# Performance work log

Hardware: AMD Instinct MI355X
Metric: run time of the kernel (lower is better)

Reference implementation:

```python
import jax, jax.numpy as jnp
import numpy as np

B, S, D, H = 4, 2048, 1024, 16
HD = D // H
DFF = 4 * D
EPS = 1e-5


def setup_inputs() -> dict:
    key = jax.random.key(0)
    ks = jax.random.split(key, 8)
    s = 0.02
    return {
        "x": jax.random.normal(ks[0], (B, S, D), dtype=jnp.float32),
        "ln1_g": jnp.ones((D,), jnp.float32),
        "ln1_b": jnp.zeros((D,), jnp.float32),
        "Wq": jax.random.normal(ks[1], (D, D), jnp.float32) * s,
        "Wk": jax.random.normal(ks[2], (D, D), jnp.float32) * s,
        "Wv": jax.random.normal(ks[3], (D, D), jnp.float32) * s,
        "Wo": jax.random.normal(ks[4], (D, D), jnp.float32) * s,
        "ln2_g": jnp.ones((D,), jnp.float32),
        "ln2_b": jnp.zeros((D,), jnp.float32),
        "W1": jax.random.normal(ks[5], (D, DFF), jnp.float32) * s,
        "b1": jnp.zeros((DFF,), jnp.float32),
        "W2": jax.random.normal(ks[6], (DFF, D), jnp.float32) * s,
        "b2": jnp.zeros((D,), jnp.float32),
    }


def _layernorm(x, g, b):
    mu = jnp.mean(x, axis=-1, keepdims=True)
    var = jnp.var(x, axis=-1, keepdims=True)
    return (x - mu) * jax.lax.rsqrt(var + EPS) * g + b


def _block(x, ln1_g, ln1_b, Wq, Wk, Wv, Wo, ln2_g, ln2_b, W1, b1, W2, b2):
    # --- attention sub-block (pre-norm) ---
    h = _layernorm(x, ln1_g, ln1_b)
    q = (h @ Wq).reshape(B, S, H, HD)
    k = (h @ Wk).reshape(B, S, H, HD)
    v = (h @ Wv).reshape(B, S, H, HD)
    scores = jnp.einsum("bqhd,bkhd->bhqk", q, k) / np.sqrt(HD).astype(np.float32)
    causal = jnp.tril(jnp.ones((S, S), dtype=bool))
    scores = jnp.where(causal, scores, -jnp.inf)
    attn = jax.nn.softmax(scores, axis=-1)  # dropout p=0 (eval)
    ctx = jnp.einsum("bhqk,bkhd->bqhd", attn, v).reshape(B, S, D)
    x = x + ctx @ Wo
    # --- FFN sub-block (pre-norm) ---
    h = _layernorm(x, ln2_g, ln2_b)
    h = jax.nn.gelu(h @ W1 + b1, approximate=False)  # torch nn.GELU() = exact erf
    return x + (h @ W2 + b2)


def reference(x, ln1_g, ln1_b, Wq, Wk, Wv, Wo, ln2_g, ln2_b, W1, b1, W2, b2):
    return _block(x, ln1_g, ln1_b, Wq, Wk, Wv, Wo, ln2_g, ln2_b, W1, b1, W2, b2)
```

## Files before the change

### kernel.cpp

```cpp
#include <hip/hip_runtime.h>
#include <hip/hip_bf16.h>
#include <math.h>

#define NB 4
#define NS 2048
#define ND 1024
#define NH 16
#define NHD 64
#define NDFF 4096
#define QKS 3072

typedef __attribute__((ext_vector_type(8))) short bf16x8;
typedef __attribute__((ext_vector_type(4))) float f32x4;
typedef __attribute__((ext_vector_type(16))) float f32x16;
typedef __attribute__((ext_vector_type(4))) short short4v;
typedef __attribute__((ext_vector_type(4))) int i32x4;

static __device__ __forceinline__ short f2b(float f) {
  union { __hip_bfloat16 b; short s; } u;
  u.b = __float2bfloat16(f);
  return u.s;
}

static __device__ __forceinline__ int cvtpk(float lo, float hi_) {
  int r;
  asm("v_cvt_pk_bf16_f32 %0, %1, %2" : "=v"(r) : "v"(lo), "v"(hi_));
  return r;
}

static __device__ __forceinline__ float pairmax(float x) {
  auto r = __builtin_amdgcn_permlane32_swap(__float_as_uint(x), __float_as_uint(x), false, false);
  return fmaxf(__uint_as_float(r[0]), __uint_as_float(r[1]));
}
static __device__ __forceinline__ float pairsum(float x) {
  auto r = __builtin_amdgcn_permlane32_swap(__float_as_uint(x), __float_as_uint(x), false, false);
  return __uint_as_float(r[0]) + __uint_as_float(r[1]);
}

__global__ __launch_bounds__(256) void ln_kernel(
    const float* __restrict__ x, const float* __restrict__ g,
    const float* __restrict__ b, short* __restrict__ out) {
  __shared__ float red[8];
  const int row = blockIdx.x;
  const int t = threadIdx.x;
  const float* xr = x + (size_t)row * ND;
  const float4 xv = *(const float4*)(xr + t * 4);
  float s = xv.x + xv.y + xv.z + xv.w;
  float ss = xv.x * xv.x + xv.y * xv.y + xv.z * xv.z + xv.w * xv.w;
#pragma unroll
  for (int m = 32; m >= 1; m >>= 1) {
    s += __shfl_xor(s, m);
    ss += __shfl_xor(ss, m);
  }
  if ((t & 63) == 0) { red[(t >> 6) * 2] = s; red[(t >> 6) * 2 + 1] = ss; }
  __syncthreads();
  s = red[0] + red[2] + red[4] + red[6];
  ss = red[1] + red[3] + red[5] + red[7];
  const float mu = s * (1.0f / ND);
  const float var = ss * (1.0f / ND) - mu * mu;
  const float rs = rsqrtf(var + 1e-5f);
  const float4 gv = *(const float4*)(g + t * 4);
  const float4 bv = *(const float4*)(b + t * 4);
  short o[4];
  o[0] = f2b((xv.x - mu) * rs * gv.x + bv.x);
  o[1] = f2b((xv.y - mu) * rs * gv.y + bv.y);
  o[2] = f2b((xv.z - mu) * rs * gv.z + bv.z);
  o[3] = f2b((xv.w - mu) * rs * gv.w + bv.w);
  *(short4v*)(out + (size_t)row * ND + t * 4) = *(short4v*)o;
}

__global__ __launch_bounds__(256) void tcast_kernel(
    const float* __restrict__ in, short* __restrict__ out, int K, int N) {
  __shared__ float tile[32][33];
  const int n0 = blockIdx.x * 32, k0 = blockIdx.y * 32;
  const int tx = threadIdx.x & 31, ty = threadIdx.x >> 5;
#pragma unroll
  for (int i = 0; i < 32; i += 8)
    tile[ty + i][tx] = in[(size_t)(k0 + ty + i) * N + n0 + tx];
  __syncthreads();
#pragma unroll
  for (int i = 0; i < 32; i += 8)
    out[(size_t)(n0 + ty + i) * K + k0 + tx] = f2b(tile[tx][ty + i]);
}

__global__ __launch_bounds__(256) void vtrans_kernel(
    const short* __restrict__ in, short* __restrict__ out) {
  __shared__ short tile[64][72];
  const int s0 = blockIdx.x * 64, bh = blockIdx.y;
  const int bb = bh >> 4, hh = bh & 15;
  const int rr = threadIdx.x >> 3, cc = (threadIdx.x & 7) * 8;
#pragma unroll
  for (int it = 0; it < 2; ++it) {
    const int r = rr + it * 32;
    *(bf16x8*)&tile[r][cc] =
        *(const bf16x8*)&in[((size_t)(bb * NS + s0 + r)) * QKS + 2048 + hh * NHD + cc];
  }
  __syncthreads();
  const size_t ob = (size_t)bh * NHD * NS;
#pragma unroll
  for (int it = 0; it < 2; ++it) {
    const int d = rr + it * 32;
    short o[8];
#pragma unroll
    for (int j = 0; j < 8; ++j) o[j] = tile[cc + j][d];
    *(bf16x8*)&out[ob + (size_t)d * NS + s0 + cc] = *(bf16x8*)o;
  }
}

__device__ __forceinline__ void gload16(const void* g, void* l) {
  __builtin_amdgcn_global_load_lds(
      (const __attribute__((address_space(1))) unsigned int*)g,
      (__attribute__((address_space(3))) unsigned int*)l, 16, 0, 0);
}

template <int BN, int EPI>
__global__ __launch_bounds__(BN * 2, 2) void gemmk_kernel(
    const short* __restrict__ A, const short* __restrict__ Bt,
    float* __restrict__ Cf, short* __restrict__ Cb,
    const float* __restrict__ bias, const float* __restrict__ res,
    int M, int N, int K) {
  constexpr int WN = BN / 64;
  constexpr int T = 128 * WN;
  constexpr int AROUNDS = 1024 / T;
  constexpr int BROUNDS = 2;
  constexpr int TS = (256 + BN) * 32;
  __shared__ short lds[3][TS];

  const int tid = threadIdx.x;
  const int l = tid & 63, w = tid >> 6;
  const int wm = w / WN, wn = w % WN;
  const int nbm = M >> 8, nbn = N / BN, nwg = nbm * nbn;
  int wg = blockIdx.x;
  wg = (wg & 7) * (nwg >> 3) + (wg >> 3);
  const int bm = wg % nbm, bn = wg / nbm;

  const int srcs = (l & 3) ^ ((l >> 2) & 3) ^ ((l >> 4) & 3);
  const short* Asrc = A + (size_t)(bm * 256 + (tid >> 2)) * K + srcs * 8;
  const short* Bsrc = Bt + (size_t)(bn * BN + (tid >> 2)) * K + srcs * 8;

  auto stage = [&](int u, int sb) {
    short* d = &lds[sb][0] + w * 512;
    const short* as = Asrc + u * 32;
    const short* bs = Bsrc + u * 32;
#pragma unroll
    for (int j = 0; j < AROUNDS; ++j)
      gload16(as + (size_t)j * (T / 4) * K, d + j * T * 8);
#pragma unroll
    for (int j = 0; j < BROUNDS; ++j)
      gload16(bs + (size_t)j * (T / 4) * K, d + 8192 + j * T * 8);
  };

  const int fr = l & 15, fg4 = l >> 4;
  int aoff[8], boff[4];
#pragma unroll
  for (int mi = 0; mi < 8; ++mi) {
    const int r = wm * 128 + mi * 16 + fr;
    aoff[mi] = r * 32 + (fg4 ^ (r & 3) ^ ((r >> 2) & 3)) * 8;
  }
#pragma unroll
  for (int nj = 0; nj < 4; ++nj) {
    const int r = wn * 64 + nj * 16 + fr;
    boff[nj] = 8192 + r * 32 + (fg4 ^ (r & 3) ^ ((r >> 2) & 3)) * 8;
  }

  f32x4 acc[8][4] = {};
  const int NT = K >> 5;
  stage(0, 0);
  stage(1, 1);
  int rb = 0;
  for (int t = 0; t < NT; ++t) {
    if (t + 1 < NT) {
      if constexpr (BN == 256)
        asm volatile("s_waitcnt vmcnt(4)\n\ts_barrier" ::: "memory");
      else
        asm volatile("s_waitcnt vmcnt(6)\n\ts_barrier" ::: "memory");
    } else {
      asm volatile("s_waitcnt vmcnt(0)\n\ts_barrier" ::: "memory");
    }
    if (t + 2 < NT) {
      int sb = rb + 2;
      if (sb >= 3) sb -= 3;
      stage(t + 2, sb);
    }
    const short* la = &lds[rb][0];
    bf16x8 af[8], bf[4];
#pragma unroll
    for (int mi = 0; mi < 8; ++mi) af[mi] = *(const bf16x8*)(la + aoff[mi]);
#pragma unroll
    for (int nj = 0; nj < 4; ++nj) bf[nj] = *(const bf16x8*)(la + boff[nj]);
    __builtin_amdgcn_s_setprio(1);
#pragma unroll
    for (int mi = 0; mi < 8; ++mi)
#pragma unroll
      for (int nj = 0; nj < 4; ++nj)
        acc[mi][nj] = __builtin_amdgcn_mfma_f32_16x16x32_bf16(af[mi], bf[nj], acc[mi][nj], 0, 0, 0);
    __builtin_amdgcn_s_setprio(0);
    if (++rb == 3) rb = 0;
  }

  const int fq = (l >> 4) * 4;
  const int wrb = bm * 256 + wm * 128;
  const int wcb = bn * BN + wn * 64;
#pragma unroll
  for (int mi = 0; mi < 8; ++mi) {
#pragma unroll
    for (int ni = 0; ni < 4; ++ni) {
#pragma unroll
      for (int rr = 0; rr < 4; ++rr) {
        const int row = wrb + mi * 16 + fq + rr;
        const int col = wcb + ni * 16 + fr;
        float v = acc[mi][ni][rr];
        if (EPI == 0) {
          Cb[(size_t)row * N + col] = f2b(v);
        } else if (EPI == 1) {
          Cf[(size_t)row * N + col] = v + res[(size_t)row * N + col];
        } else if (EPI == 2) {
          v += bias[col];
          v = 0.5f * v * (1.0f + erff(v * 0.70710678118f));
          Cb[(size_t)row * N + col] = f2b(v);
        } else {
          Cf[(size_t)row * N + col] = v + bias[col] + res[(size_t)row * N + col];
        }
      }
    }
  }
}

__global__ __launch_bounds__(256, 2) void attn_kernel(
    const short* __restrict__ qkv, const short* __restrict__ vt, short* __restrict__ ctx) {
  __shared__ short Kls[2][64 * 64];
  __shared__ short Vls[2][64 * 64];

  const int bid = blockIdx.x;
  const int bh = (bid & 7) * 8 + ((bid >> 3) & 7);
  const int cp = bid >> 6;
  const int bb = bh >> 4, hh = bh & 15;
  const int lane = threadIdx.x & 63, wave = threadIdx.x >> 6;
  const int ql = lane & 31, hi = lane >> 5;
  const int qbA = cp * 128 + wave * 32;
  const int qbB = (15 - cp) * 128 + wave * 32;

  bf16x8 qf[2][4];
#pragma unroll
  for (int hf = 0; hf < 2; ++hf) {
    const int qb0 = hf ? qbB : qbA;
    const size_t qrow = ((size_t)bb * NS + qb0 + ql) * QKS + hh * NHD;
#pragma unroll
    for (int st = 0; st < 4; ++st)
      qf[hf][st] = *(const bf16x8*)&qkv[qrow + st * 16 + hi * 8];
  }

  f32x16 acc[2][2] = {};
  float m_run[2] = {-1e37f, -1e37f};
  float l_run[2] = {0.f, 0.f};

  const int srow = lane >> 3;
  const int sslot = (lane & 7) ^ srow;
  const short* kbasep = qkv + (size_t)bb * NS * QKS + 1024 + hh * NHD + sslot * 8;
  const short* vbasep = vt + (size_t)bh * NHD * NS + sslot * 8;

  const int nkt = (16 - cp) * 2;
#pragma unroll
  for (int r = 0; r < 2; ++r) {
    const int row = r * 32 + wave * 8 + srow;
    gload16(kbasep + (size_t)row * QKS, &Kls[0][(r * 32 + wave * 8) * 64]);
    gload16(vbasep + (size_t)row * NS, &Vls[0][(r * 32 + wave * 8) * 64]);
  }

  int buf = 0;
  for (int jt = 0; jt < nkt; ++jt) {
    asm volatile("s_waitcnt vmcnt(0)\n\ts_barrier" ::: "memory");
    if (jt + 1 < nkt) {
      const int k0n = (jt + 1) * 64;
#pragma unroll
      for (int r = 0; r < 2; ++r) {
        const int row = r * 32 + wave * 8 + srow;
        gload16(kbasep + (size_t)(k0n + row) * QKS, &Kls[buf ^ 1][(r * 32 + wave * 8) * 64]);
        gload16(vbasep + (size_t)row * NS + k0n, &Vls[buf ^ 1][(r * 32 + wave * 8) * 64]);
      }
    }
    const int k0 = jt * 64;
    const short* Kb = &Kls[buf][0];
    const short* Vb = &Vls[buf][0];
#pragma unroll
    for (int ks = 0; ks < 2; ++ks) {
      const int kbase = k0 + ks * 32;
      if (kbase > qbB) continue;
      bf16x8 kf[4], vf[2][2];
      const int krow = ks * 32 + ql;
#pragma unroll
      for (int st = 0; st < 4; ++st)
        kf[st] = *(const bf16x8*)&Kb[krow * 64 + ((st * 2 + hi) ^ (krow & 7)) * 8];
#pragma unroll
      for (int db = 0; db < 2; ++db) {
        const int vrow = db * 32 + ql;
#pragma unroll
        for (int su = 0; su < 2; ++su)
          vf[db][su] =
              *(const bf16x8*)&Vb[vrow * 64 + ((ks * 4 + su * 2 + hi) ^ (vrow & 7)) * 8];
      }
#pragma unroll
      for (int hf = 0; hf < 2; ++hf) {
        const int qb0 = hf ? qbB : qbA;
        if (kbase > qb0) continue;
        const int qg = qb0 + ql;
        f32x16 s = {};
        __builtin_amdgcn_s_setprio(1);
#pragma unroll
        for (int st = 0; st < 4; ++st)
          s = __builtin_amdgcn_mfma_f32_32x32x16_bf16(kf[st], qf[hf][st], s, 0, 0, 0);
        __builtin_amdgcn_s_setprio(0);
        const bool masked = (kbase + 31 > qb0);
        float pv[16];
        float mt = -INFINITY;
#pragma unroll
        for (int r = 0; r < 16; ++r) {
          float v = s[r] * 0.125f;
          if (masked) {
            const int key = kbase + 4 * hi + (r & 3) + 8 * (r >> 2);
            v = (key > qg) ? -INFINITY : v;
          }
          pv[r] = v;
          mt = fmaxf(mt, v);
        }
        mt = pairmax(mt);
        if (!__all(mt - m_run[hf] <= 8.0f)) {
          const float mn = fmaxf(m_run[hf], mt);
          const float sc = __expf(m_run[hf] - mn);
          m_run[hf] = mn;
          l_run[hf] *= sc;
          acc[hf][0] *= sc;
          acc[hf][1] *= sc;
        }
        float pe[16];
        float lt = 0.f;
#pragma unroll
        for (int r = 0; r < 16; ++r) {
          pe[r] = __expf(fminf(pv[r] - m_run[hf], 80.0f));
          lt += pe[r];
        }
        l_run[hf] += pairsum(lt);
        bf16x8 pf[2];
#pragma unroll
        for (int su = 0; su < 2; ++su) {
          const int a0 = cvtpk(pe[su * 8 + 0], pe[su * 8 + 1]);
          const int a1 = cvtpk(pe[su * 8 + 2], pe[su * 8 + 3]);
          const int b0 = cvtpk(pe[su * 8 + 4], pe[su * 8 + 5]);
          const int b1 = cvtpk(pe[su * 8 + 6], pe[su * 8 + 7]);
          auto r0 = __builtin_amdgcn_permlane32_swap((unsigned)a0, (unsigned)b0, false, false);
          auto r1 = __builtin_amdgcn_permlane32_swap((unsigned)a1, (unsigned)b1, false, false);
          union { i32x4 w; bf16x8 v; } u;
          u.w[0] = r0[0]; u.w[1] = r1[0]; u.w[2] = r0[1]; u.w[3] = r1[1];
          pf[su] = u.v;
        }
        __builtin_amdgcn_s_setprio(1);
#pragma unroll
        for (int su = 0; su < 2; ++su) {
          acc[hf][0] = __builtin_amdgcn_mfma_f32_32x32x16_bf16(vf[0][su], pf[su], acc[hf][0], 0, 0, 0);
          acc[hf][1] = __builtin_amdgcn_mfma_f32_32x32x16_bf16(vf[1][su], pf[su], acc[hf][1], 0, 0, 0);
        }
        __builtin_amdgcn_s_setprio(0);
      }
    }
    asm volatile("s_waitcnt lgkmcnt(0)\n\ts_barrier" ::: "memory");
    buf ^= 1;
  }

#pragma unroll
  for (int hf = 0; hf < 2; ++hf) {
    const int qb0 = hf ? qbB : qbA;
    const float inv = 1.0f / l_run[hf];
    const size_t ob = ((size_t)bb * NS + qb0 + ql) * ND + hh * NHD + hi * 8;
#pragma unroll
    for (int db = 0; db < 2; ++db) {
#pragma unroll
      for (int J = 0; J < 2; ++J) {
        const int a0 = cvtpk(acc[hf][db][J * 8 + 0] * inv, acc[hf][db][J * 8 + 1] * inv);
        const int a1 = cvtpk(acc[hf][db][J * 8 + 2] * inv, acc[hf][db][J * 8 + 3] * inv);
        const int b0 = cvtpk(acc[hf][db][J * 8 + 4] * inv, acc[hf][db][J * 8 + 5] * inv);
        const int b1 = cvtpk(acc[hf][db][J * 8 + 6] * inv, acc[hf][db][J * 8 + 7] * inv);
        auto r0 = __builtin_amdgcn_permlane32_swap((unsigned)a0, (unsigned)b0, false, false);
        auto r1 = __builtin_amdgcn_permlane32_swap((unsigned)a1, (unsigned)b1, false, false);
        union { i32x4 w; bf16x8 v; } u;
        u.w[0] = r0[0]; u.w[1] = r1[0]; u.w[2] = r0[1]; u.w[3] = r1[1];
        *(bf16x8*)&ctx[ob + db * 32 + J * 16] = u.v;
      }
    }
  }
}

extern "C" void kernel_launch(void* const* d_in, const int* in_sizes, int n_in,
                              void* d_out, int out_size, void* d_ws, size_t ws_size,
                              hipStream_t stream) {
  (void)in_sizes; (void)n_in; (void)out_size; (void)ws_size;
  const float* x     = (const float*)d_in[0];
  const float* ln1_g = (const float*)d_in[1];
  const float* ln1_b = (const float*)d_in[2];
  const float* Wq    = (const float*)d_in[3];
  const float* Wk    = (const float*)d_in[4];
  const float* Wv    = (const float*)d_in[5];
  const float* Wo    = (const float*)d_in[6];
  const float* ln2_g = (const float*)d_in[7];
  const float* ln2_b = (const float*)d_in[8];
  const float* W1    = (const float*)d_in[9];
  const float* b1    = (const float*)d_in[10];
  const float* W2    = (const float*)d_in[11];
  const float* b2    = (const float*)d_in[12];
  float* out = (float*)d_out;

  char* ws = (char*)d_ws;
  const size_t MiB = 1024 * 1024;
  short* wqkvT = (short*)(ws + 0 * MiB);
  short* woT   = (short*)(ws + 6 * MiB);
  short* w1T   = (short*)(ws + 8 * MiB);
  short* w2T   = (short*)(ws + 16 * MiB);
  short* h     = (short*)(ws + 24 * MiB);
  short* ctx   = (short*)(ws + 24 * MiB);
  short* qkv   = (short*)(ws + 40 * MiB);
  short* vt    = (short*)(ws + 88 * MiB);
  short* hff   = (short*)(ws + 40 * MiB);
  float* x1    = (float*)(ws + 104 * MiB);

  tcast_kernel<<<dim3(32, 32), 256, 0, stream>>>(Wq, wqkvT, 1024, 1024);
  tcast_kernel<<<dim3(32, 32), 256, 0, stream>>>(Wk, wqkvT + 1024 * 1024, 1024, 1024);
  tcast_kernel<<<dim3(32, 32), 256, 0, stream>>>(Wv, wqkvT + 2048 * 1024, 1024, 1024);
  tcast_kernel<<<dim3(32, 32), 256, 0, stream>>>(Wo, woT, 1024, 1024);
  tcast_kernel<<<dim3(128, 32), 256, 0, stream>>>(W1, w1T, 1024, 4096);
  tcast_kernel<<<dim3(32, 128), 256, 0, stream>>>(W2, w2T, 4096, 1024);

  ln_kernel<<<8192, 256, 0, stream>>>(x, ln1_g, ln1_b, h);

  gemmk_kernel<256, 0><<<384, 512, 0, stream>>>(h, wqkvT, nullptr, qkv, nullptr, nullptr,
                                                8192, 3072, 1024);
  vtrans_kernel<<<dim3(32, 64), 256, 0, stream>>>(qkv, vt);

  attn_kernel<<<512, 256, 0, stream>>>(qkv, vt, ctx);

  gemmk_kernel<128, 1><<<256, 256, 0, stream>>>(ctx, woT, x1, nullptr, nullptr, x,
                                                8192, 1024, 1024);

  ln_kernel<<<8192, 256, 0, stream>>>(x1, ln2_g, ln2_b, h);

  gemmk_kernel<256, 2><<<512, 512, 0, stream>>>(h, w1T, nullptr, hff, b1, nullptr,
                                                8192, 4096, 1024);
  gemmk_kernel<128, 3><<<256, 256, 0, stream>>>(hff, w2T, out, nullptr, b2, x1,
                                                8192, 1024, 4096);
}
```

Before: 427.0 us.

## Restructure GEMM mainloop into double-buffered K=64 ping-pong with interleaved prefetch

```diff
diff --git a/kernel.cpp b/kernel.cpp
--- a/kernel.cpp
+++ b/kernel.cpp
@@ -114,17 +114,18 @@
 }
 
 template <int BN, int EPI>
-__global__ __launch_bounds__(BN * 2, 2) void gemmk_kernel(
+__global__ __launch_bounds__(BN == 256 ? 512 : 256, BN == 256 ? 2 : 1) void gemmp_kernel(
     const short* __restrict__ A, const short* __restrict__ Bt,
     float* __restrict__ Cf, short* __restrict__ Cb,
     const float* __restrict__ bias, const float* __restrict__ res,
     int M, int N, int K) {
   constexpr int WN = BN / 64;
-  constexpr int T = 128 * WN;
-  constexpr int AROUNDS = 1024 / T;
-  constexpr int BROUNDS = 2;
-  constexpr int TS = (256 + BN) * 32;
-  __shared__ short lds[3][TS];
+  constexpr int TPB = WN * 128;
+  constexpr int ARNDS = 16384 / (TPB * 16);
+  constexpr int BSZ = BN * 32;
+  constexpr int SZ = 16384 + BN * 64;
+  constexpr int CNT = (BN == 256) ? 4 : 6;
+  __shared__ short lds[2][SZ];
 
   const int tid = threadIdx.x;
   const int l = tid & 63, w = tid >> 6;
@@ -134,42 +135,84 @@
   wg = (wg & 7) * (nwg >> 3) + (wg >> 3);
   const int bm = wg % nbm, bn = wg / nbm;
 
-  const int srcs = (l & 3) ^ ((l >> 2) & 3) ^ ((l >> 4) & 3);
-  const short* Asrc = A + (size_t)(bm * 256 + (tid >> 2)) * K + srcs * 8;
-  const short* Bsrc = Bt + (size_t)(bn * BN + (tid >> 2)) * K + srcs * 8;
-
-  auto stage = [&](int u, int sb) {
-    short* d = &lds[sb][0] + w * 512;
-    const short* as = Asrc + u * 32;
-    const short* bs = Bsrc + u * 32;
-#pragma unroll
-    for (int j = 0; j < AROUNDS; ++j)
-      gload16(as + (size_t)j * (T / 4) * K, d + j * T * 8);
-#pragma unroll
-    for (int j = 0; j < BROUNDS; ++j)
-      gload16(bs + (size_t)j * (T / 4) * K, d + 8192 + j * T * 8);
+  const int lrow0 = w * 16 + (l >> 2);
+  const int sslot = (l & 3) ^ ((lrow0 >> 1) & 3);
+  const short* Asrc = A + (size_t)(bm * 256 + lrow0) * K + sslot * 8;
+  const short* Bsrc = Bt + (size_t)(bn * BN + lrow0) * K + sslot * 8;
+
+  auto stageA = [&](int u, int kh, short* bufb) {
+    short* d = bufb + kh * 8192 + w * 512;
+    const short* s = Asrc + (size_t)u * 64 + kh * 32;
+#pragma unroll
+    for (int j = 0; j < ARNDS; ++j)
+      gload16(s + (size_t)j * (TPB / 4) * K, d + j * TPB * 8);
   };
+  auto stageB = [&](int u, int kh, short* bufb) {
+    short* d = bufb + 16384 + kh * BSZ + w * 512;
+    const short* s = Bsrc + (size_t)u * 64 + kh * 32;
+#pragma unroll
+    for (int j = 0; j < 2; ++j)
+      gload16(s + (size_t)j * (TPB / 4) * K, d + j * TPB * 8);
+  };
 
   const int fr = l & 15, fg4 = l >> 4;
-  int aoff[8], boff[4];
+  int aoffs[8], boffs[4];
 #pragma unroll
   for (int mi = 0; mi < 8; ++mi) {
     const int r = wm * 128 + mi * 16 + fr;
-    aoff[mi] = r * 32 + (fg4 ^ (r & 3) ^ ((r >> 2) & 3)) * 8;
-  }
-#pragma unroll
-  for (int nj = 0; nj < 4; ++nj) {
-    const int r = wn * 64 + nj * 16 + fr;
-    boff[nj] = 8192 + r * 32 + (fg4 ^ (r & 3) ^ ((r >> 2) & 3)) * 8;
+    aoffs[mi] = r * 32 + ((fg4 ^ ((r >> 1) & 3)) << 3);
+  }
+#pragma unroll
+  for (int q = 0; q < 4; ++q) {
+    const int r = wn * 64 + (q >> 1) * 32 + (q & 1) * 16 + fr;
+    boffs[q] = r * 32 + ((fg4 ^ ((r >> 1) & 3)) << 3);
   }
 
   f32x4 acc[8][4] = {};
-  const int NT = K >> 5;
-  stage(0, 0);
-  stage(1, 1);
-  int rb = 0;
+  const int NT = K >> 6;
+
+  stageA(0, 0, &lds[0][0]);
+  stageB(0, 0, &lds[0][0]);
+  stageA(0, 1, &lds[0][0]);
+  stageB(0, 1, &lds[0][0]);
+  if constexpr (BN == 256)
+    asm volatile("s_waitcnt vmcnt(4)\n\ts_barrier" ::: "memory");
+  else
+    asm volatile("s_waitcnt vmcnt(6)\n\ts_barrier" ::: "memory");
+
   for (int t = 0; t < NT; ++t) {
-    if (t + 1 < NT) {
+    const short* cur = &lds[t & 1][0];
+    short* nxt = &lds[(t + 1) & 1][0];
+    const bool pf = (t + 1 < NT);
+    bf16x8 af[8], bf0, bf1;
+
+#pragma unroll
+    for (int mi = 0; mi < 8; ++mi) af[mi] = *(const bf16x8*)(cur + aoffs[mi]);
+    bf0 = *(const bf16x8*)(cur + 16384 + boffs[0]);
+    bf1 = *(const bf16x8*)(cur + 16384 + boffs[1]);
+    if (pf) stageA(t + 1, 0, nxt);
+    asm volatile("s_barrier" ::: "memory");
+    __builtin_amdgcn_s_setprio(1);
+#pragma unroll
+    for (int mi = 0; mi < 8; ++mi) {
+      acc[mi][0] = __builtin_amdgcn_mfma_f32_16x16x32_bf16(af[mi], bf0, acc[mi][0], 0, 0, 0);
+      acc[mi][1] = __builtin_amdgcn_mfma_f32_16x16x32_bf16(af[mi], bf1, acc[mi][1], 0, 0, 0);
+    }
+    __builtin_amdgcn_s_setprio(0);
+    asm volatile("s_barrier" ::: "memory");
+
+    bf0 = *(const bf16x8*)(cur + 16384 + boffs[2]);
+    bf1 = *(const bf16x8*)(cur + 16384 + boffs[3]);
+    if (pf) stageB(t + 1, 0, nxt);
+    asm volatile("s_barrier" ::: "memory");
+    __builtin_amdgcn_s_setprio(1);
+#pragma unroll
+    for (int mi = 0; mi < 8; ++mi) {
+      acc[mi][2] = __builtin_amdgcn_mfma_f32_16x16x32_bf16(af[mi], bf0, acc[mi][2], 0, 0, 0);
+      acc[mi][3] = __builtin_amdgcn_mfma_f32_16x16x32_bf16(af[mi], bf1, acc[mi][3], 0, 0, 0);
+    }
+    __builtin_amdgcn_s_setprio(0);
+    if (pf) {
       if constexpr (BN == 256)
         asm volatile("s_waitcnt vmcnt(4)\n\ts_barrier" ::: "memory");
       else
@@ -177,25 +220,39 @@
     } else {
       asm volatile("s_waitcnt vmcnt(0)\n\ts_barrier" ::: "memory");
     }
-    if (t + 2 < NT) {
-      int sb = rb + 2;
-      if (sb >= 3) sb -= 3;
-      stage(t + 2, sb);
-    }
-    const short* la = &lds[rb][0];
-    bf16x8 af[8], bf[4];
-#pragma unroll
-    for (int mi = 0; mi < 8; ++mi) af[mi] = *(const bf16x8*)(la + aoff[mi]);
-#pragma unroll
-    for (int nj = 0; nj < 4; ++nj) bf[nj] = *(const bf16x8*)(la + boff[nj]);
+
+#pragma unroll
+    for (int mi = 0; mi < 8; ++mi) af[mi] = *(const bf16x8*)(cur + 8192 + aoffs[mi]);
+    bf0 = *(const bf16x8*)(cur + 16384 + BSZ + boffs[0]);
+    bf1 = *(const bf16x8*)(cur + 16384 + BSZ + boffs[1]);
+    if (pf) stageA(t + 1, 1, nxt);
+    asm volatile("s_barrier" ::: "memory");
     __builtin_amdgcn_s_setprio(1);
 #pragma unroll
-    for (int mi = 0; mi < 8; ++mi)
-#pragma unroll
-      for (int nj = 0; nj < 4; ++nj)
-        acc[mi][nj] = __builtin_amdgcn_mfma_f32_16x16x32_bf16(af[mi], bf[nj], acc[mi][nj], 0, 0, 0);
+    for (int mi = 0; mi < 8; ++mi) {
+      acc[mi][0] = __builtin_amdgcn_mfma_f32_16x16x32_bf16(af[mi], bf0, acc[mi][0], 0, 0, 0);
+      acc[mi][1] = __builtin_amdgcn_mfma_f32_16x16x32_bf16(af[mi], bf1, acc[mi][1], 0, 0, 0);
+    }
     __builtin_amdgcn_s_setprio(0);
-    if (++rb == 3) rb = 0;
+    asm volatile("s_barrier" ::: "memory");
+
+    bf0 = *(const bf16x8*)(cur + 16384 + BSZ + boffs[2]);
+    bf1 = *(const bf16x8*)(cur + 16384 + BSZ + boffs[3]);
+    if (pf) stageB(t + 1, 1, nxt);
+    asm volatile("s_barrier" ::: "memory");
+    __builtin_amdgcn_s_setprio(1);
+#pragma unroll
+    for (int mi = 0; mi < 8; ++mi) {
+      acc[mi][2] = __builtin_amdgcn_mfma_f32_16x16x32_bf16(af[mi], bf0, acc[mi][2], 0, 0, 0);
+      acc[mi][3] = __builtin_amdgcn_mfma_f32_16x16x32_bf16(af[mi], bf1, acc[mi][3], 0, 0, 0);
+    }
+    __builtin_amdgcn_s_setprio(0);
+    if (pf) {
+      if constexpr (BN == 256)
+        asm volatile("s_waitcnt vmcnt(4)\n\ts_barrier" ::: "memory");
+      else
+        asm volatile("s_waitcnt vmcnt(6)\n\ts_barrier" ::: "memory");
+    }
   }
 
   const int fq = (l >> 4) * 4;
@@ -430,19 +487,19 @@
 
   ln_kernel<<<8192, 256, 0, stream>>>(x, ln1_g, ln1_b, h);
 
-  gemmk_kernel<256, 0><<<384, 512, 0, stream>>>(h, wqkvT, nullptr, qkv, nullptr, nullptr,
+  gemmp_kernel<256, 0><<<384, 512, 0, stream>>>(h, wqkvT, nullptr, qkv, nullptr, nullptr,
                                                 8192, 3072, 1024);
   vtrans_kernel<<<dim3(32, 64), 256, 0, stream>>>(qkv, vt);
 
   attn_kernel<<<512, 256, 0, stream>>>(qkv, vt, ctx);
 
-  gemmk_kernel<128, 1><<<256, 256, 0, stream>>>(ctx, woT, x1, nullptr, nullptr, x,
+  gemmp_kernel<128, 1><<<256, 256, 0, stream>>>(ctx, woT, x1, nullptr, nullptr, x,
                                                 8192, 1024, 1024);
 
   ln_kernel<<<8192, 256, 0, stream>>>(x1, ln2_g, ln2_b, h);
 
-  gemmk_kernel<256, 2><<<512, 512, 0, stream>>>(h, w1T, nullptr, hff, b1, nullptr,
+  gemmp_kernel<256, 2><<<512, 512, 0, stream>>>(h, w1T, nullptr, hff, b1, nullptr,
                                                 8192, 4096, 1024);
-  gemmk_kernel<128, 3><<<256, 256, 0, stream>>>(hff, w2T, out, nullptr, b2, x1,
+  gemmp_kernel<128, 3><<<256, 256, 0, stream>>>(hff, w2T, out, nullptr, b2, x1,
                                                 8192, 1024, 4096);
 }
```

Measured after the change: 445.5 us. 4.3% more time.

## Rewrite GEMM kernel with 4-stage LDS pipeline and 512-thread blocks

Applied to the files above, without the earlier changes.

```diff
diff --git a/kernel.cpp b/kernel.cpp
--- a/kernel.cpp
+++ b/kernel.cpp
@@ -114,95 +114,115 @@
 }
 
 template <int BN, int EPI>
-__global__ __launch_bounds__(BN * 2, 2) void gemmk_kernel(
+__global__ __launch_bounds__(512, 2) void gemmr_kernel(
     const short* __restrict__ A, const short* __restrict__ Bt,
     float* __restrict__ Cf, short* __restrict__ Cb,
     const float* __restrict__ bias, const float* __restrict__ res,
     int M, int N, int K) {
-  constexpr int WN = BN / 64;
-  constexpr int T = 128 * WN;
-  constexpr int AROUNDS = 1024 / T;
-  constexpr int BROUNDS = 2;
-  constexpr int TS = (256 + BN) * 32;
-  __shared__ short lds[3][TS];
-
-  const int tid = threadIdx.x;
-  const int l = tid & 63, w = tid >> 6;
-  const int wm = w / WN, wn = w % WN;
+  constexpr int MI = (BN == 256) ? 8 : 4;
+  constexpr int NWN = (BN == 256) ? 4 : 2;
+  constexpr int ABUF = 8192;
+  constexpr int TS = ABUF + BN * 32;
+  __shared__ short lds[4][TS];
+
+  const int tid = threadIdx.x, l = tid & 63, w = tid >> 6;
+  const int wm = w / NWN, wn = w % NWN;
   const int nbm = M >> 8, nbn = N / BN, nwg = nbm * nbn;
   int wg = blockIdx.x;
   wg = (wg & 7) * (nwg >> 3) + (wg >> 3);
-  const int bm = wg % nbm, bn = wg / nbm;
-
-  const int srcs = (l & 3) ^ ((l >> 2) & 3) ^ ((l >> 4) & 3);
-  const short* Asrc = A + (size_t)(bm * 256 + (tid >> 2)) * K + srcs * 8;
-  const short* Bsrc = Bt + (size_t)(bn * BN + (tid >> 2)) * K + srcs * 8;
-
-  auto stage = [&](int u, int sb) {
-    short* d = &lds[sb][0] + w * 512;
-    const short* as = Asrc + u * 32;
-    const short* bs = Bsrc + u * 32;
-#pragma unroll
-    for (int j = 0; j < AROUNDS; ++j)
-      gload16(as + (size_t)j * (T / 4) * K, d + j * T * 8);
-#pragma unroll
-    for (int j = 0; j < BROUNDS; ++j)
-      gload16(bs + (size_t)j * (T / 4) * K, d + 8192 + j * T * 8);
-  };
+  const int bm = wg / nbn, bn = wg % nbn;
+
+  const int lrow = tid >> 2;
+  const int sslot = (l & 3) ^ ((lrow >> 1) & 3);
+  const short* Asrc = A + (size_t)(bm * 256 + lrow) * K + sslot * 8;
+  const short* Bsrc = Bt + (size_t)(bn * BN + lrow) * K + sslot * 8;
+  const int ldst = w * 512;
 
   const int fr = l & 15, fg4 = l >> 4;
-  int aoff[8], boff[4];
-#pragma unroll
-  for (int mi = 0; mi < 8; ++mi) {
-    const int r = wm * 128 + mi * 16 + fr;
-    aoff[mi] = r * 32 + (fg4 ^ (r & 3) ^ ((r >> 2) & 3)) * 8;
+  int aoff[MI], boff[4];
+#pragma unroll
+  for (int mi = 0; mi < MI; ++mi) {
+    const int r = wm * (MI * 16) + mi * 16 + fr;
+    aoff[mi] = r * 32 + ((fg4 ^ ((r >> 1) & 3)) << 3);
   }
 #pragma unroll
   for (int nj = 0; nj < 4; ++nj) {
     const int r = wn * 64 + nj * 16 + fr;
-    boff[nj] = 8192 + r * 32 + (fg4 ^ (r & 3) ^ ((r >> 2) & 3)) * 8;
-  }
-
-  f32x4 acc[8][4] = {};
+    boff[nj] = ABUF + r * 32 + ((fg4 ^ ((r >> 1) & 3)) << 3);
+  }
+
+  auto stageAB = [&](int t, short* buf) {
+    const short* sa = Asrc + t * 32;
+    gload16(sa, buf + ldst);
+    gload16(sa + (size_t)128 * K, buf + 4096 + ldst);
+    const short* sb = Bsrc + t * 32;
+    gload16(sb, buf + ABUF + ldst);
+    if constexpr (BN == 256) gload16(sb + (size_t)128 * K, buf + ABUF + 4096 + ldst);
+  };
+
+  f32x4 acc[MI][4] = {};
   const int NT = K >> 5;
-  stage(0, 0);
-  stage(1, 1);
-  int rb = 0;
+
+  stageAB(0, lds[0]);
+  stageAB(1, lds[1]);
+  stageAB(2, lds[2]);
+  if constexpr (BN == 256)
+    asm volatile("s_waitcnt vmcnt(8)\n\ts_barrier" ::: "memory");
+  else
+    asm volatile("s_waitcnt vmcnt(6)\n\ts_barrier" ::: "memory");
+
   for (int t = 0; t < NT; ++t) {
-    if (t + 1 < NT) {
+    const short* cur = &lds[t & 3][0];
+    short* pbuf = &lds[(t + 3) & 3][0];
+    const bool st = (t + 3 < NT);
+    bf16x8 bfr[4], af[4];
+#pragma unroll
+    for (int nj = 0; nj < 4; ++nj) bfr[nj] = *(const bf16x8*)(cur + boff[nj]);
+#pragma unroll
+    for (int mi = 0; mi < 4; ++mi) af[mi] = *(const bf16x8*)(cur + aoff[mi]);
+    if (st) stageAB(t + 3, pbuf);
+    asm volatile("s_barrier" ::: "memory");
+    __builtin_amdgcn_s_setprio(1);
+#pragma unroll
+    for (int mi = 0; mi < 4; ++mi)
+#pragma unroll
+      for (int nj = 0; nj < 4; ++nj)
+        acc[mi][nj] = __builtin_amdgcn_mfma_f32_16x16x32_bf16(af[mi], bfr[nj], acc[mi][nj], 0, 0, 0);
+    __builtin_amdgcn_s_setprio(0);
+    if constexpr (BN == 256) {
+      asm volatile("s_barrier" ::: "memory");
+#pragma unroll
+      for (int mi = 0; mi < 4; ++mi) af[mi] = *(const bf16x8*)(cur + aoff[4 + mi]);
+      asm volatile("s_barrier" ::: "memory");
+      __builtin_amdgcn_s_setprio(1);
+#pragma unroll
+      for (int mi = 0; mi < 4; ++mi)
+#pragma unroll
+        for (int nj = 0; nj < 4; ++nj)
+          acc[4 + mi][nj] =
+              __builtin_amdgcn_mfma_f32_16x16x32_bf16(af[mi], bfr[nj], acc[4 + mi][nj], 0, 0, 0);
+      __builtin_amdgcn_s_setprio(0);
+    }
+    if (t + 3 < NT) {
+      if constexpr (BN == 256)
+        asm volatile("s_waitcnt vmcnt(8)\n\ts_barrier" ::: "memory");
+      else
+        asm volatile("s_waitcnt vmcnt(6)\n\ts_barrier" ::: "memory");
+    } else if (t + 2 < NT) {
       if constexpr (BN == 256)
         asm volatile("s_waitcnt vmcnt(4)\n\ts_barrier" ::: "memory");
       else
-        asm volatile("s_waitcnt vmcnt(6)\n\ts_barrier" ::: "memory");
-    } else {
+        asm volatile("s_waitcnt vmcnt(3)\n\ts_barrier" ::: "memory");
+    } else if (t + 1 < NT) {
       asm volatile("s_waitcnt vmcnt(0)\n\ts_barrier" ::: "memory");
     }
-    if (t + 2 < NT) {
-      int sb = rb + 2;
-      if (sb >= 3) sb -= 3;
-      stage(t + 2, sb);
-    }
-    const short* la = &lds[rb][0];
-    bf16x8 af[8], bf[4];
-#pragma unroll
-    for (int mi = 0; mi < 8; ++mi) af[mi] = *(const bf16x8*)(la + aoff[mi]);
-#pragma unroll
-    for (int nj = 0; nj < 4; ++nj) bf[nj] = *(const bf16x8*)(la + boff[nj]);
-    __builtin_amdgcn_s_setprio(1);
-#pragma unroll
-    for (int mi = 0; mi < 8; ++mi)
-#pragma unroll
-      for (int nj = 0; nj < 4; ++nj)
-        acc[mi][nj] = __builtin_amdgcn_mfma_f32_16x16x32_bf16(af[mi], bf[nj], acc[mi][nj], 0, 0, 0);
-    __builtin_amdgcn_s_setprio(0);
-    if (++rb == 3) rb = 0;
   }
 
   const int fq = (l >> 4) * 4;
-  const int wrb = bm * 256 + wm * 128;
+  const int wrb = bm * 256 + wm * (MI * 16);
   const int wcb = bn * BN + wn * 64;
 #pragma unroll
-  for (int mi = 0; mi < 8; ++mi) {
+  for (int mi = 0; mi < MI; ++mi) {
 #pragma unroll
     for (int ni = 0; ni < 4; ++ni) {
 #pragma unroll
@@ -430,19 +450,19 @@
 
   ln_kernel<<<8192, 256, 0, stream>>>(x, ln1_g, ln1_b, h);
 
-  gemmk_kernel<256, 0><<<384, 512, 0, stream>>>(h, wqkvT, nullptr, qkv, nullptr, nullptr,
+  gemmr_kernel<128, 0><<<768, 512, 0, stream>>>(h, wqkvT, nullptr, qkv, nullptr, nullptr,
                                                 8192, 3072, 1024);
   vtrans_kernel<<<dim3(32, 64), 256, 0, stream>>>(qkv, vt);
 
   attn_kernel<<<512, 256, 0, stream>>>(qkv, vt, ctx);
 
-  gemmk_kernel<128, 1><<<256, 256, 0, stream>>>(ctx, woT, x1, nullptr, nullptr, x,
+  gemmr_kernel<128, 1><<<256, 512, 0, stream>>>(ctx, woT, x1, nullptr, nullptr, x,
                                                 8192, 1024, 1024);
 
   ln_kernel<<<8192, 256, 0, stream>>>(x1, ln2_g, ln2_b, h);
 
-  gemmk_kernel<256, 2><<<512, 512, 0, stream>>>(h, w1T, nullptr, hff, b1, nullptr,
+  gemmr_kernel<256, 2><<<512, 512, 0, stream>>>(h, w1T, nullptr, hff, b1, nullptr,
                                                 8192, 4096, 1024);
-  gemmk_kernel<128, 3><<<256, 256, 0, stream>>>(hff, w2T, out, nullptr, b2, x1,
+  gemmr_kernel<128, 3><<<256, 512, 0, stream>>>(hff, w2T, out, nullptr, b2, x1,
                                                 8192, 1024, 4096);
 }
```

Result: faster. 387.9 us (-9.2%).
